# Performance work log

Measured on AMD Instinct MI355X. Metric: run time of the kernel, lower is better.

## Reference

```python
import jax, jax.numpy as jnp
import numpy as np

LATENT = 10
MAXLEN = 80
DT = 0.1
STEPS = int(round(1.0 / DT))
HIDDEN = 32
BATCH = 512


def _score_fn(xt_bld, time_b1, W1, b1, W2, b2):
    # score_model: flatten (B, L, D) -> concat time -> Dense(32, relu) -> Dense(D)
    B = xt_bld.shape[0]
    h = jnp.concatenate([xt_bld.reshape(B, -1), time_b1], axis=-1)  # (B, L*D+1)
    h = jax.nn.relu(h @ W1 + b1)
    return h @ W2 + b2  # (B, D)


def setup_inputs() -> dict:
    key = jax.random.key(0)
    k1, k2, k3, k4 = jax.random.split(key, 4)
    fan_in = MAXLEN * LATENT + 1  # 801
    z_mean = jax.random.normal(k1, (BATCH, MAXLEN, LATENT), jnp.float32)
    z_log_var = 0.1 * jax.random.normal(k2, (BATCH, MAXLEN, LATENT), jnp.float32)
    W1 = jax.random.normal(k3, (fan_in, HIDDEN), jnp.float32) / np.sqrt(fan_in)
    b1 = jnp.zeros((HIDDEN,), jnp.float32)
    W2 = jax.random.normal(k4, (HIDDEN, LATENT), jnp.float32) / np.sqrt(HIDDEN)
    b2 = jnp.zeros((LATENT,), jnp.float32)
    return {"z_mean": z_mean, "z_log_var": z_log_var, "W1": W1, "b1": b1, "W2": W2, "b2": b2}


def _diffusion_loss(z_mean, z_log_var, W1, b1, W2, b2):
    B = z_mean.shape[0]
    sigma = jnp.exp(z_log_var)                    # ez_log_var in train_step
    mu_tr = jnp.transpose(z_mean, (1, 0, 2))      # (L, B, D)
    sigma_tr = jnp.transpose(sigma, (1, 0, 2))    # (L, B, D)
    zero = jnp.zeros((1, B, LATENT), mu_tr.dtype)
    full_mu_ext = jnp.concatenate([zero, mu_tr], axis=0)       # (L+1, B, D)
    full_sigma_ext = jnp.concatenate([zero, sigma_tr], axis=0)  # (L+1, B, D)
    noise_keys = jax.random.split(jax.random.key(1337), MAXLEN * (STEPS + 1)).reshape(MAXLEN, STEPS + 1)

    def diffusion_step(i, mu_i, sigma_i, keys):
        # mask_below_target_step: keep rows < i
        mask = (jnp.arange(MAXLEN) < i).astype(mu_tr.dtype)[:, None, None]
        masked_mu = mu_tr * mask                                   # (L, B, D)
        times = i.astype(jnp.float32) + jnp.arange(STEPS, dtype=jnp.float32) * DT
        sigma_std = jnp.sqrt(sigma_i)                              # (B, D)
        x0 = mu_i + sigma_std * jax.random.normal(keys[0], (B, LATENT))

        def body(xt, xs):
            t, k = xs
            t_idx = jnp.floor(t).astype(jnp.int32)
            next_mu = jax.lax.dynamic_index_in_dim(full_mu_ext, t_idx + 1, 0, keepdims=False)
            next_sigma = jax.lax.dynamic_index_in_dim(full_sigma_ext, t_idx + 1, 0, keepdims=False)
            one_hot = jax.nn.one_hot(t_idx, MAXLEN, dtype=xt.dtype)     # (L,)
            score_in = masked_mu + one_hot[:, None, None] * xt[None]    # (L, B, D)
            score_in = jnp.transpose(score_in, (1, 0, 2))               # (B, L, D)
            time_col = jnp.full((B, 1), t, xt.dtype)
            score = _score_fn(score_in, time_col, W1, b1, W2, b2)       # (B, D)
            logdx = -(xt - next_mu) / jnp.sqrt(next_sigma)
            err = jnp.abs(logdx - score)
            dW = jax.random.normal(k, (B, LATENT)) * jnp.sqrt(DT)
            xt = xt + 0.5 * jnp.square(sigma_std) * score + sigma_std * dW
            return xt, err

        xt_final, errs = jax.lax.scan(body, x0, (times, keys[1:]))
        return xt_final, errs.sum(axis=0)  # tf.reduce_sum(error, axis=0)

    seq, err = jax.vmap(diffusion_step)(jnp.arange(MAXLEN), mu_tr, sigma_tr, noise_keys)
    sequence = jnp.transpose(seq, (1, 0, 2))       # (B, L, D)
    score_error = jnp.transpose(err, (1, 0, 2))    # (B, L, D)
    return sequence, score_error


def reference(z_mean, z_log_var, W1, b1, W2, b2):
    return _diffusion_loss(z_mean, z_log_var, W1, b1, W2, b2)
```

## Files before the change

kernel.cpp:

```cpp
#include <hip/hip_runtime.h>
#include <stdint.h>

#define LATENT 10
#define MAXLEN 80
#define STEPS  10
#define HIDDEN 32
#define BATCH  512
#define NSEG   16
#define SEGL   5
#define CPB    16
#define TPB    128

#define SCP_STRIDE 84
#define US_STRIDE  12

__device__ __forceinline__ void tf2x32(uint32_t k0, uint32_t k1,
                                       uint32_t x0, uint32_t x1,
                                       uint32_t& o0, uint32_t& o1) {
  uint32_t ks2 = k0 ^ k1 ^ 0x1BD11BDAu;
  uint32_t v0 = x0 + k0;
  uint32_t v1 = x1 + k1;
#define TF_R(rot) { v0 += v1; v1 = (v1 << (rot)) | (v1 >> (32 - (rot))); v1 ^= v0; }
  TF_R(13) TF_R(15) TF_R(26) TF_R(6)
  v0 += k1;  v1 += ks2 + 1u;
  TF_R(17) TF_R(29) TF_R(16) TF_R(24)
  v0 += ks2; v1 += k0 + 2u;
  TF_R(13) TF_R(15) TF_R(26) TF_R(6)
  v0 += k0;  v1 += k1 + 3u;
  TF_R(17) TF_R(29) TF_R(16) TF_R(24)
  v0 += k1;  v1 += ks2 + 4u;
  TF_R(13) TF_R(15) TF_R(26) TF_R(6)
  v0 += ks2; v1 += k0 + 5u;
#undef TF_R
  o0 = v0; o1 = v1;
}

__device__ __forceinline__ float bits_to_normal(uint32_t bits) {
  const float lo = -0.99999994f;
  float f = __uint_as_float((bits >> 9) | 0x3f800000u) - 1.0f;
  float u = fmaf(f, 2.0f, lo);
  u = fmaxf(u, lo);
  float w = -__logf(fmaf(-u, u, 1.0f));
  float p;
  if (w < 5.0f) {
    w -= 2.5f;
    p = 2.81022636e-08f;
    p = fmaf(p, w, 3.43273939e-07f);
    p = fmaf(p, w, -3.5233877e-06f);
    p = fmaf(p, w, -4.39150654e-06f);
    p = fmaf(p, w, 0.00021858087f);
    p = fmaf(p, w, -0.00125372503f);
    p = fmaf(p, w, -0.00417768164f);
    p = fmaf(p, w, 0.246640727f);
    p = fmaf(p, w, 1.50140941f);
  } else {
    w = sqrtf(w) - 3.0f;
    p = -0.000200214257f;
    p = fmaf(p, w, 0.000100950558f);
    p = fmaf(p, w, 0.00134934322f);
    p = fmaf(p, w, -0.00367342844f);
    p = fmaf(p, w, 0.00573950773f);
    p = fmaf(p, w, -0.0076224613f);
    p = fmaf(p, w, 0.00943887047f);
    p = fmaf(p, w, 1.00167406f);
    p = fmaf(p, w, 2.83297682f);
  }
  return 1.4142135623730951f * (p * u);
}

__global__ __launch_bounds__(256) void k_seg(
    const float* __restrict__ zmean, const float* __restrict__ W1,
    float* __restrict__ segtot) {
  int id = blockIdx.x * 256 + threadIdx.x;
  int s = id >> 14;
  int r = id & 16383;
  int b = r >> 5, j = r & 31;
  float pf0 = 0.0f, pf1 = 0.0f;
#pragma unroll
  for (int t = 0; t < SEGL; ++t) {
    int l = s * SEGL + t;
    const float2* mrow = (const float2*)(zmean + (b * MAXLEN + l) * LATENT);
    float2 m0 = mrow[0], m1 = mrow[1], m2 = mrow[2], m3 = mrow[3], m4 = mrow[4];
    const float* wl = W1 + (l * LATENT) * HIDDEN + j;
    pf0 = fmaf(m0.x, wl[0 * HIDDEN], pf0);
    pf1 = fmaf(m0.y, wl[1 * HIDDEN], pf1);
    pf0 = fmaf(m1.x, wl[2 * HIDDEN], pf0);
    pf1 = fmaf(m1.y, wl[3 * HIDDEN], pf1);
    pf0 = fmaf(m2.x, wl[4 * HIDDEN], pf0);
    pf1 = fmaf(m2.y, wl[5 * HIDDEN], pf1);
    pf0 = fmaf(m3.x, wl[6 * HIDDEN], pf0);
    pf1 = fmaf(m3.y, wl[7 * HIDDEN], pf1);
    pf0 = fmaf(m4.x, wl[8 * HIDDEN], pf0);
    pf1 = fmaf(m4.y, wl[9 * HIDDEN], pf1);
  }
  segtot[(s * BATCH + b) * HIDDEN + j] = pf0 + pf1;
}

__global__ __launch_bounds__(TPB) void k_chain(
    const float* __restrict__ zmean, const float* __restrict__ zlv,
    const float* __restrict__ W1, const float* __restrict__ b1v,
    const float* __restrict__ W2, const float* __restrict__ b2v,
    const float* __restrict__ segtot,
    float* __restrict__ outSeq, float* __restrict__ outErr) {
  __shared__ float nrmS[(STEPS + 1) * LATENT * CPB];
  __shared__ uint32_t skk[2 * (STEPS + 1)];
  __shared__ float shS[CPB * LATENT];
  __shared__ float scP[CPB * SCP_STRIDE];
  __shared__ float uS[CPB * US_STRIDE];

  const int tid = threadIdx.x;
  const int i = blockIdx.x >> 5;
  const int b0 = (blockIdx.x & 31) << 4;

  if (tid < (STEPS + 1)) {
    uint32_t a, c;
    tf2x32(0u, 1337u, 0u, (uint32_t)(i * (STEPS + 1) + tid), a, c);
    skk[2 * tid] = a; skk[2 * tid + 1] = c;
  }
  for (int t = tid; t < CPB * LATENT; t += TPB) {
    int c_ = t / LATENT, d_ = t - c_ * LATENT;
    shS[t] = 0.5f * sqrtf(expf(zlv[((b0 + c_) * MAXLEN + i) * LATENT + d_]));
  }
  __syncthreads();

  const float SQRT_DT = 0.31622776601683794f;
#define GEN_DRAW(IDX)                                                        \
  {                                                                          \
    int c_ = (IDX) & (CPB - 1), n_ = (IDX) >> 4;                             \
    int k_ = (n_ * 205) >> 11;                                               \
    int d_ = n_ - k_ * 10;                                                   \
    uint32_t o0_, o1_;                                                       \
    tf2x32(skk[2 * k_], skk[2 * k_ + 1], 0u,                                 \
           (uint32_t)((b0 + c_) * LATENT + d_), o0_, o1_);                   \
    float v_ = bits_to_normal(o0_ ^ o1_);                                    \
    nrmS[n_ * CPB + c_] = (n_ < LATENT) ? v_ : v_ * SQRT_DT;                 \
  }
#pragma unroll
  for (int rr = 0; rr < 13; ++rr) GEN_DRAW(rr * TPB + tid);
  if (tid < (STEPS + 1) * LATENT * CPB - 13 * TPB) GEN_DRAW(13 * TPB + tid);
#undef GEN_DRAW
  __syncthreads();

  const int r = tid & 7;
  const int jb = r * 4;
  const int cloc = tid >> 3;
  const int b = b0 + cloc;

  const float* rowT = W1 + (MAXLEN * LATENT) * HIDDEN;
  float pf[4], wT[4];
  const float fi = (float)i;
#pragma unroll
  for (int k = 0; k < 4; ++k) {
    wT[k] = rowT[jb + k];
    pf[k] = fmaf(fi, wT[k], b1v[jb + k]);
  }
  const int fs = i / SEGL;
  for (int s2 = 0; s2 < fs; ++s2) {
    float4 t0 = *(const float4*)(segtot + ((size_t)s2 * BATCH + b) * HIDDEN + jb);
    pf[0] += t0.x; pf[1] += t0.y; pf[2] += t0.z; pf[3] += t0.w;
  }
  for (int l = fs * SEGL; l < i; ++l) {
    const float2* mrow = (const float2*)(zmean + (b * MAXLEN + l) * LATENT);
    const float* wl = W1 + (l * LATENT) * HIDDEN + jb;
#pragma unroll
    for (int p = 0; p < 5; ++p) {
      float2 m = mrow[p];
      float4 wa = *(const float4*)(wl + (2 * p) * HIDDEN);
      float4 wb = *(const float4*)(wl + (2 * p + 1) * HIDDEN);
      pf[0] = fmaf(m.x, wa.x, pf[0]); pf[1] = fmaf(m.x, wa.y, pf[1]);
      pf[2] = fmaf(m.x, wa.z, pf[2]); pf[3] = fmaf(m.x, wa.w, pf[3]);
      pf[0] = fmaf(m.y, wb.x, pf[0]); pf[1] = fmaf(m.y, wb.y, pf[1]);
      pf[2] = fmaf(m.y, wb.z, pf[2]); pf[3] = fmaf(m.y, wb.w, pf[3]);
    }
  }

  const int base = (b * MAXLEN + i) * LATENT;
  float w1s[LATENT][4];
  {
    const float2* zm = (const float2*)(zmean + base);
    const float2* shp = (const float2*)(shS + cloc * LATENT);
    const float* W1i = W1 + (i * LATENT) * HIDDEN + jb;
#pragma unroll
    for (int p = 0; p < 5; ++p) {
      float2 m = zm[p];
      float2 sh = shp[p];
      float s0 = sh.x + sh.x;
      float s1 = sh.y + sh.y;
      float4 wa = *(const float4*)(W1i + (2 * p) * HIDDEN);
      float4 wb = *(const float4*)(W1i + (2 * p + 1) * HIDDEN);
      pf[0] = fmaf(m.x, wa.x, pf[0]); pf[1] = fmaf(m.x, wa.y, pf[1]);
      pf[2] = fmaf(m.x, wa.z, pf[2]); pf[3] = fmaf(m.x, wa.w, pf[3]);
      pf[0] = fmaf(m.y, wb.x, pf[0]); pf[1] = fmaf(m.y, wb.y, pf[1]);
      pf[2] = fmaf(m.y, wb.z, pf[2]); pf[3] = fmaf(m.y, wb.w, pf[3]);
      w1s[2 * p][0] = s0 * wa.x; w1s[2 * p][1] = s0 * wa.y;
      w1s[2 * p][2] = s0 * wa.z; w1s[2 * p][3] = s0 * wa.w;
      w1s[2 * p + 1][0] = s1 * wb.x; w1s[2 * p + 1][1] = s1 * wb.y;
      w1s[2 * p + 1][2] = s1 * wb.z; w1s[2 * p + 1][3] = s1 * wb.w;
    }
  }

  float sh0 = shS[cloc * LATENT + r];
  float b2o0 = b2v[r];
  float u0o = nrmS[r * CPB + cloc];
  float e0 = 0.0f;
  float sh1 = 0.0f, b2o1 = 0.0f, u1o = 0.0f, e1 = 0.0f;
  if (r < 2) {
    sh1 = shS[cloc * LATENT + 8 + r];
    b2o1 = b2v[8 + r];
    u1o = nrmS[(8 + r) * CPB + cloc];
  }
  {
    float* uw = uS + cloc * US_STRIDE;
    uw[r] = u0o;
    if (r < 2) uw[8 + r] = u1o;
  }

  const float* W2q = W2 + jb * LATENT;
  float* scw = scP + cloc * SCP_STRIDE + r;
  const float* scrd0 = scP + cloc * SCP_STRIDE + r * 8;
  const float* scrd1 = scP + cloc * SCP_STRIDE + (8 + r) * 8;
  const float2* urd = (const float2*)(uS + cloc * US_STRIDE);
  const float* ndp = nrmS + LATENT * CPB + cloc;

  for (int s = 0; s < STEPS; ++s) {
    float2 ua = urd[0], ub = urd[1], uc = urd[2], ud = urd[3], ue = urd[4];

    const float ts = (float)s * 0.1f;
    float h[4];
#pragma unroll
    for (int k = 0; k < 4; ++k) h[k] = fmaf(ts, wT[k], pf[k]);
#define ACC(d, val) { h[0] = fmaf((val), w1s[d][0], h[0]); h[1] = fmaf((val), w1s[d][1], h[1]); \
                      h[2] = fmaf((val), w1s[d][2], h[2]); h[3] = fmaf((val), w1s[d][3], h[3]); }
    ACC(0, ua.x) ACC(1, ua.y) ACC(2, ub.x) ACC(3, ub.y) ACC(4, uc.x)
    ACC(5, uc.y) ACC(6, ud.x) ACC(7, ud.y) ACC(8, ue.x) ACC(9, ue.y)
#undef ACC

    float sc[LATENT];
    {
      float hj = fmaxf(h[0], 0.0f);
      const float2* w2r = (const float2*)(W2q);
#pragma unroll
      for (int p = 0; p < 5; ++p) {
        float2 w = w2r[p];
        sc[2 * p] = hj * w.x; sc[2 * p + 1] = hj * w.y;
      }
    }
#pragma unroll
    for (int k = 1; k < 4; ++k) {
      float hj = fmaxf(h[k], 0.0f);
      const float2* w2r = (const float2*)(W2q + k * LATENT);
#pragma unroll
      for (int p = 0; p < 5; ++p) {
        float2 w = w2r[p];
        sc[2 * p] = fmaf(hj, w.x, sc[2 * p]);
        sc[2 * p + 1] = fmaf(hj, w.y, sc[2 * p + 1]);
      }
    }

#pragma unroll
    for (int d = 0; d < LATENT; ++d) scw[d * 8] = sc[d];

    {
      float4 lo = *(const float4*)(scrd0);
      float4 hi = *(const float4*)(scrd0 + 4);
      float ssum = ((lo.x + lo.y) + (lo.z + lo.w)) +
                   ((hi.x + hi.y) + (hi.z + hi.w));
      float st = ssum + b2o0;
      float ndv = ndp[s * (LATENT * CPB) + r * CPB];
      e0 += fabsf(u0o + st);
      u0o = u0o + fmaf(sh0, st, ndv);
    }
    if (r < 2) {
      float4 lo = *(const float4*)(scrd1);
      float4 hi = *(const float4*)(scrd1 + 4);
      float ssum = ((lo.x + lo.y) + (lo.z + lo.w)) +
                   ((hi.x + hi.y) + (hi.z + hi.w));
      float st = ssum + b2o1;
      float ndv = ndp[s * (LATENT * CPB) + (8 + r) * CPB];
      e1 += fabsf(u1o + st);
      u1o = u1o + fmaf(sh1, st, ndv);
    }

    {
      float* uw = uS + cloc * US_STRIDE;
      uw[r] = u0o;
      if (r < 2) uw[8 + r] = u1o;
    }
  }

  {
    float sd0 = sh0 + sh0;
    outSeq[base + r] = fmaf(sd0, u0o, zmean[base + r]);
    outErr[base + r] = e0;
    if (r < 2) {
      float sd1 = sh1 + sh1;
      outSeq[base + 8 + r] = fmaf(sd1, u1o, zmean[base + 8 + r]);
      outErr[base + 8 + r] = e1;
    }
  }
}

__global__ __launch_bounds__(64) void k_mono(
    const float* __restrict__ zmean, const float* __restrict__ zlv,
    const float* __restrict__ W1, const float* __restrict__ b1v,
    const float* __restrict__ W2, const float* __restrict__ b2v,
    float* __restrict__ outSeq, float* __restrict__ outErr) {
  int i = blockIdx.x >> 3;
  int b = ((blockIdx.x & 7) << 6) + threadIdx.x;
  float pref[HIDDEN];
#pragma unroll
  for (int j = 0; j < HIDDEN; ++j) pref[j] = 0.0f;
  for (int l = 0; l < i; ++l) {
    const float* mrow = zmean + (b * MAXLEN + l) * LATENT;
    const float* wrow = W1 + (l * LATENT) * HIDDEN;
#pragma unroll
    for (int d = 0; d < LATENT; ++d) {
      float m = mrow[d];
#pragma unroll
      for (int j = 0; j < HIDDEN; ++j) pref[j] = fmaf(m, wrow[d * HIDDEN + j], pref[j]);
    }
  }
  const int base = (b * MAXLEN + i) * LATENT;
  float mu[LATENT], sstd[LATENT], xt[LATENT], errs[LATENT];
#pragma unroll
  for (int d = 0; d < LATENT; ++d) {
    mu[d] = zmean[base + d];
    sstd[d] = sqrtf(expf(zlv[base + d]));
  }
  float n0[LATENT];
  {
    uint32_t a, c;
    tf2x32(0u, 1337u, 0u, (uint32_t)(i * (STEPS + 1)), a, c);
#pragma unroll
    for (int d = 0; d < LATENT; ++d) {
      uint32_t o0, o1;
      tf2x32(a, c, 0u, (uint32_t)(b * LATENT + d), o0, o1);
      n0[d] = bits_to_normal(o0 ^ o1);
    }
  }
#pragma unroll
  for (int d = 0; d < LATENT; ++d) { xt[d] = mu[d] + sstd[d] * n0[d]; errs[d] = 0.0f; }
  const float* rowT  = W1 + (MAXLEN * LATENT) * HIDDEN;
  const float* rowsI = W1 + (i * LATENT) * HIDDEN;
  const float SQRT_DT = 0.31622776601683794f;
  for (int s = 0; s < STEPS; ++s) {
    float t = (float)i + (float)s * 0.1f;
    float h[HIDDEN];
#pragma unroll
    for (int j = 0; j < HIDDEN; ++j) h[j] = pref[j];
#pragma unroll
    for (int d = 0; d < LATENT; ++d) {
      float xd = xt[d];
      const float* row = rowsI + d * HIDDEN;
#pragma unroll
      for (int j = 0; j < HIDDEN; ++j) h[j] = fmaf(xd, row[j], h[j]);
    }
    float sc[LATENT];
#pragma unroll
    for (int d = 0; d < LATENT; ++d) sc[d] = b2v[d];
#pragma unroll
    for (int j = 0; j < HIDDEN; ++j) {
      float hj = fmaf(t, rowT[j], h[j]) + b1v[j];
      hj = fmaxf(hj, 0.0f);
      const float* w2r = W2 + j * LATENT;
#pragma unroll
      for (int d = 0; d < LATENT; ++d) sc[d] = fmaf(hj, w2r[d], sc[d]);
    }
    float nd[LATENT];
    {
      uint32_t a, c;
      tf2x32(0u, 1337u, 0u, (uint32_t)(i * (STEPS + 1) + s + 1), a, c);
#pragma unroll
      for (int d = 0; d < LATENT; ++d) {
        uint32_t o0, o1;
        tf2x32(a, c, 0u, (uint32_t)(b * LATENT + d), o0, o1);
        nd[d] = bits_to_normal(o0 ^ o1);
      }
    }
#pragma unroll
    for (int d = 0; d < LATENT; ++d) {
      float logdx = -(xt[d] - mu[d]) / sstd[d];
      errs[d] += fabsf(logdx - sc[d]);
      float dW = nd[d] * SQRT_DT;
      xt[d] = xt[d] + (0.5f * (sstd[d] * sstd[d])) * sc[d] + sstd[d] * dW;
    }
  }
#pragma unroll
  for (int d = 0; d < LATENT; ++d) {
    outSeq[base + d] = xt[d];
    outErr[base + d] = errs[d];
  }
}

extern "C" void kernel_launch(void* const* d_in, const int* in_sizes, int n_in,
                              void* d_out, int out_size, void* d_ws, size_t ws_size,
                              hipStream_t stream) {
  (void)in_sizes; (void)n_in; (void)out_size;
  const float* zmean = (const float*)d_in[0];
  const float* zlv   = (const float*)d_in[1];
  const float* W1    = (const float*)d_in[2];
  const float* b1v   = (const float*)d_in[3];
  const float* W2    = (const float*)d_in[4];
  const float* b2v   = (const float*)d_in[5];
  float* outSeq = (float*)d_out;
  float* outErr = outSeq + (size_t)BATCH * MAXLEN * LATENT;

  const size_t segBytes = (size_t)NSEG * BATCH * HIDDEN * sizeof(float);

  if (ws_size >= segBytes) {
    float* segtot = (float*)d_ws;
    hipLaunchKernelGGL(k_seg, dim3(NSEG * BATCH * HIDDEN / 256), dim3(256), 0, stream,
                       zmean, W1, segtot);
    hipLaunchKernelGGL(k_chain, dim3(MAXLEN * (BATCH / CPB)), dim3(TPB), 0, stream,
                       zmean, zlv, W1, b1v, W2, b2v, segtot, outSeq, outErr);
  } else {
    hipLaunchKernelGGL(k_mono, dim3(MAXLEN * 8), dim3(64), 0, stream,
                       zmean, zlv, W1, b1v, W2, b2v, outSeq, outErr);
  }
}
```

Baseline: 100.8 us.

## Move Threefry normal generation into the precompute kernel via workspace buffer

Random normal draws that k_chain used to compute per block (Threefry plus an inverse-erf polynomial) are now produced by extra blocks of the first kernel, which is renamed k_pre, and written to a workspace buffer. k_chain then loads them with float4 reads into shared memory, overlapped with the zlv setup, and drops one barrier. The aim is to take the RNG compute off the k_chain critical path and run it in parallel with the segment-sum blocks. In exchange it adds about 11 MB of global write and read traffic and needs a larger workspace, otherwise the fallback path runs.

Measured after the change: 106.4 us. 5.6% more time.

```diff
diff --git a/kernel.cpp b/kernel.cpp
--- a/kernel.cpp
+++ b/kernel.cpp
@@ -13,6 +13,8 @@
 
 #define SCP_STRIDE 84
 #define US_STRIDE  12
+
+#define RNG_STRIDE 1792
 
 __device__ __forceinline__ void tf2x32(uint32_t k0, uint32_t k1,
                                        uint32_t x0, uint32_t x1,
@@ -68,42 +70,73 @@
   return 1.4142135623730951f * (p * u);
 }
 
-__global__ __launch_bounds__(256) void k_seg(
+__global__ __launch_bounds__(256) void k_pre(
     const float* __restrict__ zmean, const float* __restrict__ W1,
-    float* __restrict__ segtot) {
-  int id = blockIdx.x * 256 + threadIdx.x;
-  int s = id >> 14;
-  int r = id & 16383;
-  int b = r >> 5, j = r & 31;
-  float pf0 = 0.0f, pf1 = 0.0f;
-#pragma unroll
-  for (int t = 0; t < SEGL; ++t) {
-    int l = s * SEGL + t;
-    const float2* mrow = (const float2*)(zmean + (b * MAXLEN + l) * LATENT);
-    float2 m0 = mrow[0], m1 = mrow[1], m2 = mrow[2], m3 = mrow[3], m4 = mrow[4];
-    const float* wl = W1 + (l * LATENT) * HIDDEN + j;
-    pf0 = fmaf(m0.x, wl[0 * HIDDEN], pf0);
-    pf1 = fmaf(m0.y, wl[1 * HIDDEN], pf1);
-    pf0 = fmaf(m1.x, wl[2 * HIDDEN], pf0);
-    pf1 = fmaf(m1.y, wl[3 * HIDDEN], pf1);
-    pf0 = fmaf(m2.x, wl[4 * HIDDEN], pf0);
-    pf1 = fmaf(m2.y, wl[5 * HIDDEN], pf1);
-    pf0 = fmaf(m3.x, wl[6 * HIDDEN], pf0);
-    pf1 = fmaf(m3.y, wl[7 * HIDDEN], pf1);
-    pf0 = fmaf(m4.x, wl[8 * HIDDEN], pf0);
-    pf1 = fmaf(m4.y, wl[9 * HIDDEN], pf1);
-  }
-  segtot[(s * BATCH + b) * HIDDEN + j] = pf0 + pf1;
+    float* __restrict__ segtot, float* __restrict__ rng) {
+  __shared__ uint32_t skk[2 * (STEPS + 1)];
+  const int bid = blockIdx.x;
+  const int tid = threadIdx.x;
+
+  if (bid < 1024) {
+    int id = bid * 256 + tid;
+    int s = id >> 14;
+    int r = id & 16383;
+    int b = r >> 5, j = r & 31;
+    float pf0 = 0.0f, pf1 = 0.0f;
+#pragma unroll
+    for (int t = 0; t < SEGL; ++t) {
+      int l = s * SEGL + t;
+      const float2* mrow = (const float2*)(zmean + (b * MAXLEN + l) * LATENT);
+      float2 m0 = mrow[0], m1 = mrow[1], m2 = mrow[2], m3 = mrow[3], m4 = mrow[4];
+      const float* wl = W1 + (l * LATENT) * HIDDEN + j;
+      pf0 = fmaf(m0.x, wl[0 * HIDDEN], pf0);
+      pf1 = fmaf(m0.y, wl[1 * HIDDEN], pf1);
+      pf0 = fmaf(m1.x, wl[2 * HIDDEN], pf0);
+      pf1 = fmaf(m1.y, wl[3 * HIDDEN], pf1);
+      pf0 = fmaf(m2.x, wl[4 * HIDDEN], pf0);
+      pf1 = fmaf(m2.y, wl[5 * HIDDEN], pf1);
+      pf0 = fmaf(m3.x, wl[6 * HIDDEN], pf0);
+      pf1 = fmaf(m3.y, wl[7 * HIDDEN], pf1);
+      pf0 = fmaf(m4.x, wl[8 * HIDDEN], pf0);
+      pf1 = fmaf(m4.y, wl[9 * HIDDEN], pf1);
+    }
+    segtot[(s * BATCH + b) * HIDDEN + j] = pf0 + pf1;
+  } else {
+    const int cb = bid - 1024;
+    const int i = cb >> 5;
+    const int b0 = (cb & 31) << 4;
+    if (tid < (STEPS + 1)) {
+      uint32_t a, c;
+      tf2x32(0u, 1337u, 0u, (uint32_t)(i * (STEPS + 1) + tid), a, c);
+      skk[2 * tid] = a; skk[2 * tid + 1] = c;
+    }
+    __syncthreads();
+    const float SQRT_DT = 0.31622776601683794f;
+    float* dst = rng + (size_t)cb * RNG_STRIDE;
+#pragma unroll
+    for (int it = 0; it < 7; ++it) {
+      int slot = it * 256 + tid;
+      if (slot < (STEPS + 1) * LATENT * CPB) {
+        int c_ = slot & (CPB - 1), n_ = slot >> 4;
+        int k_ = (n_ * 205) >> 11;
+        int d_ = n_ - k_ * 10;
+        uint32_t o0_, o1_;
+        tf2x32(skk[2 * k_], skk[2 * k_ + 1], 0u,
+               (uint32_t)((b0 + c_) * LATENT + d_), o0_, o1_);
+        float v_ = bits_to_normal(o0_ ^ o1_);
+        dst[slot] = (n_ < LATENT) ? v_ : v_ * SQRT_DT;
+      }
+    }
+  }
 }
 
 __global__ __launch_bounds__(TPB) void k_chain(
     const float* __restrict__ zmean, const float* __restrict__ zlv,
     const float* __restrict__ W1, const float* __restrict__ b1v,
     const float* __restrict__ W2, const float* __restrict__ b2v,
-    const float* __restrict__ segtot,
+    const float* __restrict__ segtot, const float* __restrict__ rng,
     float* __restrict__ outSeq, float* __restrict__ outErr) {
-  __shared__ float nrmS[(STEPS + 1) * LATENT * CPB];
-  __shared__ uint32_t skk[2 * (STEPS + 1)];
+  __shared__ __align__(16) float nrmS[RNG_STRIDE];
   __shared__ float shS[CPB * LATENT];
   __shared__ float scP[CPB * SCP_STRIDE];
   __shared__ float uS[CPB * US_STRIDE];
@@ -112,33 +145,22 @@
   const int i = blockIdx.x >> 5;
   const int b0 = (blockIdx.x & 31) << 4;
 
-  if (tid < (STEPS + 1)) {
-    uint32_t a, c;
-    tf2x32(0u, 1337u, 0u, (uint32_t)(i * (STEPS + 1) + tid), a, c);
-    skk[2 * tid] = a; skk[2 * tid + 1] = c;
-  }
+  const float4* src4 = (const float4*)(rng + (size_t)blockIdx.x * RNG_STRIDE);
+  float4* nrm4 = (float4*)nrmS;
+  float4 st0 = src4[0 * TPB + tid];
+  float4 st1 = src4[1 * TPB + tid];
+  float4 st2 = src4[2 * TPB + tid];
+  float4 st3 = make_float4(0.0f, 0.0f, 0.0f, 0.0f);
+  if (tid < 64) st3 = src4[3 * TPB + tid];
+
   for (int t = tid; t < CPB * LATENT; t += TPB) {
     int c_ = t / LATENT, d_ = t - c_ * LATENT;
     shS[t] = 0.5f * sqrtf(expf(zlv[((b0 + c_) * MAXLEN + i) * LATENT + d_]));
   }
-  __syncthreads();
-
-  const float SQRT_DT = 0.31622776601683794f;
-#define GEN_DRAW(IDX)                                                        \
-  {                                                                          \
-    int c_ = (IDX) & (CPB - 1), n_ = (IDX) >> 4;                             \
-    int k_ = (n_ * 205) >> 11;                                               \
-    int d_ = n_ - k_ * 10;                                                   \
-    uint32_t o0_, o1_;                                                       \
-    tf2x32(skk[2 * k_], skk[2 * k_ + 1], 0u,                                 \
-           (uint32_t)((b0 + c_) * LATENT + d_), o0_, o1_);                   \
-    float v_ = bits_to_normal(o0_ ^ o1_);                                    \
-    nrmS[n_ * CPB + c_] = (n_ < LATENT) ? v_ : v_ * SQRT_DT;                 \
-  }
-#pragma unroll
-  for (int rr = 0; rr < 13; ++rr) GEN_DRAW(rr * TPB + tid);
-  if (tid < (STEPS + 1) * LATENT * CPB - 13 * TPB) GEN_DRAW(13 * TPB + tid);
-#undef GEN_DRAW
+  nrm4[0 * TPB + tid] = st0;
+  nrm4[1 * TPB + tid] = st1;
+  nrm4[2 * TPB + tid] = st2;
+  if (tid < 64) nrm4[3 * TPB + tid] = st3;
   __syncthreads();
 
   const int r = tid & 7;
@@ -406,13 +428,15 @@
   float* outErr = outSeq + (size_t)BATCH * MAXLEN * LATENT;
 
   const size_t segBytes = (size_t)NSEG * BATCH * HIDDEN * sizeof(float);
-
-  if (ws_size >= segBytes) {
+  const size_t rngBytes = (size_t)MAXLEN * (BATCH / CPB) * RNG_STRIDE * 4;
+
+  if (ws_size >= segBytes + rngBytes) {
     float* segtot = (float*)d_ws;
-    hipLaunchKernelGGL(k_seg, dim3(NSEG * BATCH * HIDDEN / 256), dim3(256), 0, stream,
-                       zmean, W1, segtot);
+    float* rng = (float*)d_ws + segBytes / sizeof(float);
+    hipLaunchKernelGGL(k_pre, dim3(1024 + MAXLEN * (BATCH / CPB)), dim3(256), 0, stream,
+                       zmean, W1, segtot, rng);
     hipLaunchKernelGGL(k_chain, dim3(MAXLEN * (BATCH / CPB)), dim3(TPB), 0, stream,
-                       zmean, zlv, W1, b1v, W2, b2v, segtot, outSeq, outErr);
+                       zmean, zlv, W1, b1v, W2, b2v, segtot, rng, outSeq, outErr);
   } else {
     hipLaunchKernelGGL(k_mono, dim3(MAXLEN * 8), dim3(64), 0, stream,
                        zmean, zlv, W1, b1v, W2, b2v, outSeq, outErr);
```

## Precompute per-position hidden prefix sums in a separate kernel before the chain

Applied to the files above, without the earlier changes.

Adds a k_pf kernel that builds, for every position, batch and hidden unit, the full masked-prefix pre-activation (bias, time term, segment totals, in-segment prefix and the current row's mean). It writes them to a workspace table, so k_chain loads one float4 instead of looping over up to 79 rows of z_mean and W1. This removes the load imbalance across position blocks in the chain kernel. The cost is an extra launch and a 5 MB write plus read through workspace, and the path now needs more workspace to be taken.

New measurement: 105.9 us. 5.0% more time.

```diff
diff --git a/kernel.cpp b/kernel.cpp
--- a/kernel.cpp
+++ b/kernel.cpp
@@ -13,6 +13,7 @@
 
 #define SCP_STRIDE 84
 #define US_STRIDE  12
+
 
 __device__ __forceinline__ void tf2x32(uint32_t k0, uint32_t k1,
                                        uint32_t x0, uint32_t x1,
@@ -96,11 +97,61 @@
   segtot[(s * BATCH + b) * HIDDEN + j] = pf0 + pf1;
 }
 
+__global__ __launch_bounds__(256) void k_pf(
+    const float* __restrict__ zmean, const float* __restrict__ W1,
+    const float* __restrict__ b1v, const float* __restrict__ segtot,
+    float* __restrict__ pfT) {
+  int id = blockIdx.x * 256 + threadIdx.x;
+  int sseg = id >> 14;
+  int r = id & 16383;
+  int b = r >> 5, j = r & 31;
+  const int lbase = sseg * SEGL;
+
+  const float wTj = W1[(MAXLEN * LATENT) * HIDDEN + j];
+  const float b1j = b1v[j];
+
+  float muS[SEGL][LATENT], wS[SEGL][LATENT];
+#pragma unroll
+  for (int o = 0; o < SEGL; ++o) {
+    const float2* mrow = (const float2*)(zmean + (b * MAXLEN + lbase + o) * LATENT);
+#pragma unroll
+    for (int p = 0; p < 5; ++p) {
+      float2 m = mrow[p];
+      muS[o][2 * p] = m.x; muS[o][2 * p + 1] = m.y;
+    }
+    const float* wl = W1 + ((lbase + o) * LATENT) * HIDDEN + j;
+#pragma unroll
+    for (int d = 0; d < LATENT; ++d) wS[o][d] = wl[d * HIDDEN];
+  }
+
+  float acc[SEGL];
+#pragma unroll
+  for (int o = 0; o < SEGL; ++o) acc[o] = fmaf((float)(lbase + o), wTj, b1j);
+
+  for (int s2 = 0; s2 < sseg; ++s2) {
+    float sv = segtot[((size_t)s2 * BATCH + b) * HIDDEN + j];
+    acc[0] += sv; acc[1] += sv; acc[2] += sv; acc[3] += sv; acc[4] += sv;
+  }
+
+#pragma unroll
+  for (int o = 0; o < SEGL; ++o) {
+#pragma unroll
+    for (int lp = 0; lp <= o; ++lp) {
+#pragma unroll
+      for (int d = 0; d < LATENT; ++d)
+        acc[o] = fmaf(muS[lp][d], wS[lp][d], acc[o]);
+    }
+  }
+
+#pragma unroll
+  for (int o = 0; o < SEGL; ++o)
+    pfT[((size_t)(lbase + o) * BATCH + b) * HIDDEN + j] = acc[o];
+}
+
 __global__ __launch_bounds__(TPB) void k_chain(
     const float* __restrict__ zmean, const float* __restrict__ zlv,
-    const float* __restrict__ W1, const float* __restrict__ b1v,
-    const float* __restrict__ W2, const float* __restrict__ b2v,
-    const float* __restrict__ segtot,
+    const float* __restrict__ W1, const float* __restrict__ b2v,
+    const float* __restrict__ W2, const float* __restrict__ pfT,
     float* __restrict__ outSeq, float* __restrict__ outErr) {
   __shared__ float nrmS[(STEPS + 1) * LATENT * CPB];
   __shared__ uint32_t skk[2 * (STEPS + 1)];
@@ -148,50 +199,25 @@
 
   const float* rowT = W1 + (MAXLEN * LATENT) * HIDDEN;
   float pf[4], wT[4];
-  const float fi = (float)i;
-#pragma unroll
-  for (int k = 0; k < 4; ++k) {
-    wT[k] = rowT[jb + k];
-    pf[k] = fmaf(fi, wT[k], b1v[jb + k]);
-  }
-  const int fs = i / SEGL;
-  for (int s2 = 0; s2 < fs; ++s2) {
-    float4 t0 = *(const float4*)(segtot + ((size_t)s2 * BATCH + b) * HIDDEN + jb);
-    pf[0] += t0.x; pf[1] += t0.y; pf[2] += t0.z; pf[3] += t0.w;
-  }
-  for (int l = fs * SEGL; l < i; ++l) {
-    const float2* mrow = (const float2*)(zmean + (b * MAXLEN + l) * LATENT);
-    const float* wl = W1 + (l * LATENT) * HIDDEN + jb;
-#pragma unroll
-    for (int p = 0; p < 5; ++p) {
-      float2 m = mrow[p];
-      float4 wa = *(const float4*)(wl + (2 * p) * HIDDEN);
-      float4 wb = *(const float4*)(wl + (2 * p + 1) * HIDDEN);
-      pf[0] = fmaf(m.x, wa.x, pf[0]); pf[1] = fmaf(m.x, wa.y, pf[1]);
-      pf[2] = fmaf(m.x, wa.z, pf[2]); pf[3] = fmaf(m.x, wa.w, pf[3]);
-      pf[0] = fmaf(m.y, wb.x, pf[0]); pf[1] = fmaf(m.y, wb.y, pf[1]);
-      pf[2] = fmaf(m.y, wb.z, pf[2]); pf[3] = fmaf(m.y, wb.w, pf[3]);
-    }
-  }
+  {
+    float4 pv = *(const float4*)(pfT + ((size_t)i * BATCH + b) * HIDDEN + jb);
+    pf[0] = pv.x; pf[1] = pv.y; pf[2] = pv.z; pf[3] = pv.w;
+  }
+#pragma unroll
+  for (int k = 0; k < 4; ++k) wT[k] = rowT[jb + k];
 
   const int base = (b * MAXLEN + i) * LATENT;
   float w1s[LATENT][4];
   {
-    const float2* zm = (const float2*)(zmean + base);
     const float2* shp = (const float2*)(shS + cloc * LATENT);
     const float* W1i = W1 + (i * LATENT) * HIDDEN + jb;
 #pragma unroll
     for (int p = 0; p < 5; ++p) {
-      float2 m = zm[p];
       float2 sh = shp[p];
       float s0 = sh.x + sh.x;
       float s1 = sh.y + sh.y;
       float4 wa = *(const float4*)(W1i + (2 * p) * HIDDEN);
       float4 wb = *(const float4*)(W1i + (2 * p + 1) * HIDDEN);
-      pf[0] = fmaf(m.x, wa.x, pf[0]); pf[1] = fmaf(m.x, wa.y, pf[1]);
-      pf[2] = fmaf(m.x, wa.z, pf[2]); pf[3] = fmaf(m.x, wa.w, pf[3]);
-      pf[0] = fmaf(m.y, wb.x, pf[0]); pf[1] = fmaf(m.y, wb.y, pf[1]);
-      pf[2] = fmaf(m.y, wb.z, pf[2]); pf[3] = fmaf(m.y, wb.w, pf[3]);
       w1s[2 * p][0] = s0 * wa.x; w1s[2 * p][1] = s0 * wa.y;
       w1s[2 * p][2] = s0 * wa.z; w1s[2 * p][3] = s0 * wa.w;
       w1s[2 * p + 1][0] = s1 * wb.x; w1s[2 * p + 1][1] = s1 * wb.y;
@@ -406,13 +432,17 @@
   float* outErr = outSeq + (size_t)BATCH * MAXLEN * LATENT;
 
   const size_t segBytes = (size_t)NSEG * BATCH * HIDDEN * sizeof(float);
-
-  if (ws_size >= segBytes) {
+  const size_t pfBytes  = (size_t)MAXLEN * BATCH * HIDDEN * sizeof(float);
+
+  if (ws_size >= segBytes + pfBytes) {
     float* segtot = (float*)d_ws;
+    float* pfT    = (float*)d_ws + segBytes / sizeof(float);
     hipLaunchKernelGGL(k_seg, dim3(NSEG * BATCH * HIDDEN / 256), dim3(256), 0, stream,
                        zmean, W1, segtot);
+    hipLaunchKernelGGL(k_pf, dim3(NSEG * BATCH * HIDDEN / 256), dim3(256), 0, stream,
+                       zmean, W1, b1v, segtot, pfT);
     hipLaunchKernelGGL(k_chain, dim3(MAXLEN * (BATCH / CPB)), dim3(TPB), 0, stream,
-                       zmean, zlv, W1, b1v, W2, b2v, segtot, outSeq, outErr);
+                       zmean, zlv, W1, b2v, W2, pfT, outSeq, outErr);
   } else {
     hipLaunchKernelGGL(k_mono, dim3(MAXLEN * 8), dim3(64), 0, stream,
                        zmean, zlv, W1, b1v, W2, b2v, outSeq, outErr);
```

## Make prologue RNG and sigma setup wave-local to drop block barriers

Applied to the files above, without the earlier changes.

Each 64-lane wavefront now computes its own copy of the step keys and the sigma and noise values for its own 8 batch columns. This removes the two block-wide __syncthreads in the prologue. The global prefix accumulation of W1 partial sums is moved ahead of the Threefry noise generation so memory latency can overlap with the RNG arithmetic. The per-step noise loads are hoisted to the top of the step loop. The cost is redundant key computation per wave and more reliance on wave-level ordering of shared-memory writes and reads without explicit barriers.

Result: no change. 99.29 us (median of 2 runs) (-1.5%).

```diff
diff --git a/kernel.cpp b/kernel.cpp
--- a/kernel.cpp
+++ b/kernel.cpp
@@ -103,48 +103,42 @@
     const float* __restrict__ segtot,
     float* __restrict__ outSeq, float* __restrict__ outErr) {
   __shared__ float nrmS[(STEPS + 1) * LATENT * CPB];
-  __shared__ uint32_t skk[2 * (STEPS + 1)];
+  __shared__ uint32_t skkW[2][2 * (STEPS + 1)];
   __shared__ float shS[CPB * LATENT];
   __shared__ float scP[CPB * SCP_STRIDE];
   __shared__ float uS[CPB * US_STRIDE];
 
   const int tid = threadIdx.x;
+  const int lane = tid & 63;
+  const int wid = tid >> 6;
   const int i = blockIdx.x >> 5;
   const int b0 = (blockIdx.x & 31) << 4;
 
-  if (tid < (STEPS + 1)) {
+  if (lane < (STEPS + 1)) {
     uint32_t a, c;
-    tf2x32(0u, 1337u, 0u, (uint32_t)(i * (STEPS + 1) + tid), a, c);
-    skk[2 * tid] = a; skk[2 * tid + 1] = c;
-  }
-  for (int t = tid; t < CPB * LATENT; t += TPB) {
-    int c_ = t / LATENT, d_ = t - c_ * LATENT;
-    shS[t] = 0.5f * sqrtf(expf(zlv[((b0 + c_) * MAXLEN + i) * LATENT + d_]));
-  }
-  __syncthreads();
-
-  const float SQRT_DT = 0.31622776601683794f;
-#define GEN_DRAW(IDX)                                                        \
-  {                                                                          \
-    int c_ = (IDX) & (CPB - 1), n_ = (IDX) >> 4;                             \
-    int k_ = (n_ * 205) >> 11;                                               \
-    int d_ = n_ - k_ * 10;                                                   \
-    uint32_t o0_, o1_;                                                       \
-    tf2x32(skk[2 * k_], skk[2 * k_ + 1], 0u,                                 \
-           (uint32_t)((b0 + c_) * LATENT + d_), o0_, o1_);                   \
-    float v_ = bits_to_normal(o0_ ^ o1_);                                    \
-    nrmS[n_ * CPB + c_] = (n_ < LATENT) ? v_ : v_ * SQRT_DT;                 \
-  }
-#pragma unroll
-  for (int rr = 0; rr < 13; ++rr) GEN_DRAW(rr * TPB + tid);
-  if (tid < (STEPS + 1) * LATENT * CPB - 13 * TPB) GEN_DRAW(13 * TPB + tid);
-#undef GEN_DRAW
-  __syncthreads();
+    tf2x32(0u, 1337u, 0u, (uint32_t)(i * (STEPS + 1) + lane), a, c);
+    skkW[wid][2 * lane] = a; skkW[wid][2 * lane + 1] = c;
+  }
+
+  {
+    int c8 = lane / 10, d_ = lane - c8 * 10;
+    int cc = (wid << 3) + c8;
+    shS[cc * LATENT + d_] =
+        0.5f * sqrtf(expf(zlv[((b0 + cc) * MAXLEN + i) * LATENT + d_]));
+    if (lane < 16) {
+      int f2 = 64 + lane;
+      int c8b = f2 / 10, d2 = f2 - c8b * 10;
+      int cc2 = (wid << 3) + c8b;
+      shS[cc2 * LATENT + d2] =
+          0.5f * sqrtf(expf(zlv[((b0 + cc2) * MAXLEN + i) * LATENT + d2]));
+    }
+  }
 
   const int r = tid & 7;
   const int jb = r * 4;
   const int cloc = tid >> 3;
   const int b = b0 + cloc;
+  const int base = (b * MAXLEN + i) * LATENT;
 
   const float* rowT = W1 + (MAXLEN * LATENT) * HIDDEN;
   float pf[4], wT[4];
@@ -173,25 +167,52 @@
       pf[2] = fmaf(m.y, wb.z, pf[2]); pf[3] = fmaf(m.y, wb.w, pf[3]);
     }
   }
-
-  const int base = (b * MAXLEN + i) * LATENT;
-  float w1s[LATENT][4];
   {
     const float2* zm = (const float2*)(zmean + base);
-    const float2* shp = (const float2*)(shS + cloc * LATENT);
     const float* W1i = W1 + (i * LATENT) * HIDDEN + jb;
 #pragma unroll
     for (int p = 0; p < 5; ++p) {
       float2 m = zm[p];
-      float2 sh = shp[p];
-      float s0 = sh.x + sh.x;
-      float s1 = sh.y + sh.y;
       float4 wa = *(const float4*)(W1i + (2 * p) * HIDDEN);
       float4 wb = *(const float4*)(W1i + (2 * p + 1) * HIDDEN);
       pf[0] = fmaf(m.x, wa.x, pf[0]); pf[1] = fmaf(m.x, wa.y, pf[1]);
       pf[2] = fmaf(m.x, wa.z, pf[2]); pf[3] = fmaf(m.x, wa.w, pf[3]);
       pf[0] = fmaf(m.y, wb.x, pf[0]); pf[1] = fmaf(m.y, wb.y, pf[1]);
       pf[2] = fmaf(m.y, wb.z, pf[2]); pf[3] = fmaf(m.y, wb.w, pf[3]);
+    }
+  }
+
+  const float SQRT_DT = 0.31622776601683794f;
+  {
+    const uint32_t* skw = skkW[wid];
+#pragma unroll
+    for (int t = 0; t < 14; ++t) {
+      int idx = t * 64 + lane;
+      int n_ = idx >> 3;
+      if (n_ < (STEPS + 1) * LATENT) {
+        int c_ = (wid << 3) + (idx & 7);
+        int k_ = (n_ * 205) >> 11;
+        int d_ = n_ - k_ * 10;
+        uint32_t o0_, o1_;
+        tf2x32(skw[2 * k_], skw[2 * k_ + 1], 0u,
+               (uint32_t)((b0 + c_) * LATENT + d_), o0_, o1_);
+        float v_ = bits_to_normal(o0_ ^ o1_);
+        nrmS[n_ * CPB + c_] = (n_ < LATENT) ? v_ : v_ * SQRT_DT;
+      }
+    }
+  }
+
+  float w1s[LATENT][4];
+  {
+    const float2* shp = (const float2*)(shS + cloc * LATENT);
+    const float* W1i = W1 + (i * LATENT) * HIDDEN + jb;
+#pragma unroll
+    for (int p = 0; p < 5; ++p) {
+      float2 sh = shp[p];
+      float s0 = sh.x + sh.x;
+      float s1 = sh.y + sh.y;
+      float4 wa = *(const float4*)(W1i + (2 * p) * HIDDEN);
+      float4 wb = *(const float4*)(W1i + (2 * p + 1) * HIDDEN);
       w1s[2 * p][0] = s0 * wa.x; w1s[2 * p][1] = s0 * wa.y;
       w1s[2 * p][2] = s0 * wa.z; w1s[2 * p][3] = s0 * wa.w;
       w1s[2 * p + 1][0] = s1 * wb.x; w1s[2 * p + 1][1] = s1 * wb.y;
@@ -224,6 +245,9 @@
 
   for (int s = 0; s < STEPS; ++s) {
     float2 ua = urd[0], ub = urd[1], uc = urd[2], ud = urd[3], ue = urd[4];
+    float ndv0 = ndp[s * (LATENT * CPB) + r * CPB];
+    float ndv1 = 0.0f;
+    if (r < 2) ndv1 = ndp[s * (LATENT * CPB) + (8 + r) * CPB];
 
     const float ts = (float)s * 0.1f;
     float h[4];
@@ -266,9 +290,8 @@
       float ssum = ((lo.x + lo.y) + (lo.z + lo.w)) +
                    ((hi.x + hi.y) + (hi.z + hi.w));
       float st = ssum + b2o0;
-      float ndv = ndp[s * (LATENT * CPB) + r * CPB];
       e0 += fabsf(u0o + st);
-      u0o = u0o + fmaf(sh0, st, ndv);
+      u0o = u0o + fmaf(sh0, st, ndv0);
     }
     if (r < 2) {
       float4 lo = *(const float4*)(scrd1);
@@ -276,9 +299,8 @@
       float ssum = ((lo.x + lo.y) + (lo.z + lo.w)) +
                    ((hi.x + hi.y) + (hi.z + hi.w));
       float st = ssum + b2o1;
-      float ndv = ndp[s * (LATENT * CPB) + (8 + r) * CPB];
       e1 += fabsf(u1o + st);
-      u1o = u1o + fmaf(sh1, st, ndv);
+      u1o = u1o + fmaf(sh1, st, ndv1);
     }
 
     {
```
